# Kernel tuning notes

Measured on AMD Instinct MI355X. Metric: run time of the kernel, lower is better.

The kernel has to match this reference:

```python
import jax, jax.numpy as jnp
import numpy as np

N_NODES = 100000
N_FEATS = 2048
HIDDEN = 64
N_LABELS = 40
NNZ_FEAT = 2500000   # ~25 nonzero features per node
N_EDGES = 1600000    # avg degree 16 (directed COO entries)


def setup_inputs() -> dict:
    key = jax.random.key(0)
    ks = jax.random.split(key, 10)

    # sparse feature matrix [N_NODES, N_FEATS] in COO form
    f_rows = jax.random.randint(ks[0], (NNZ_FEAT,), 0, N_NODES)
    f_cols = jax.random.randint(ks[1], (NNZ_FEAT,), 0, N_FEATS)
    feature_indices = jnp.stack([f_rows, f_cols]).astype(jnp.int64)
    feature_values = jax.random.uniform(ks[2], (NNZ_FEAT,), dtype=jnp.float32)

    # random graph edges + self loops, then D^-1/2 (A+I) D^-1/2 normalization
    e_rows = jax.random.randint(ks[3], (N_EDGES,), 0, N_NODES)
    e_cols = jax.random.randint(ks[4], (N_EDGES,), 0, N_NODES)
    loops = jnp.arange(N_NODES)
    rows = jnp.concatenate([e_rows, loops])
    cols = jnp.concatenate([e_cols, loops])
    deg = jax.ops.segment_sum(jnp.ones_like(rows, dtype=jnp.float32), rows,
                              num_segments=N_NODES)
    deg = deg + jax.ops.segment_sum(jnp.ones_like(cols, dtype=jnp.float32), cols,
                                    num_segments=N_NODES)
    d_inv_sqrt = jax.lax.rsqrt(jnp.maximum(deg * 0.5, 1.0))
    edge_indices = jnp.stack([rows, cols]).astype(jnp.int64)
    edge_weights = d_inv_sqrt[rows] * d_inv_sqrt[cols]

    # xavier-uniform weights, uniform(-1/sqrt(out), 1/sqrt(out)) biases
    lim1 = np.sqrt(6.0 / (N_FEATS + HIDDEN))
    W1 = jax.random.uniform(ks[5], (N_FEATS, HIDDEN), jnp.float32, -lim1, lim1)
    b1 = jax.random.uniform(ks[6], (HIDDEN,), jnp.float32,
                            -1.0 / np.sqrt(HIDDEN), 1.0 / np.sqrt(HIDDEN))
    lim2 = np.sqrt(6.0 / (HIDDEN + N_LABELS))
    W2 = jax.random.uniform(ks[7], (HIDDEN, N_LABELS), jnp.float32, -lim2, lim2)
    b2 = jax.random.uniform(ks[8], (N_LABELS,), jnp.float32,
                            -1.0 / np.sqrt(N_LABELS), 1.0 / np.sqrt(N_LABELS))

    return {"feature_indices": feature_indices, "feature_values": feature_values,
            "edge_indices": edge_indices, "edge_weights": edge_weights,
            "W1": W1, "b1": b1, "W2": W2, "b2": b2}


def _spmm(rows, cols, vals, dense):
    # (sparse [N, M]) @ (dense [M, D]) -> [N, D]
    return jax.ops.segment_sum(vals[:, None] * dense[cols], rows,
                               num_segments=N_NODES)


def reference(feature_indices, feature_values, edge_indices, edge_weights,
              W1, b1, W2, b2):
    f_rows, f_cols = feature_indices
    e_rows, e_cols = edge_indices

    # layer 1: sparse feature SpMM + bias
    h = _spmm(f_rows, f_cols, feature_values, W1) + b1        # [N, HIDDEN]
    # propagate with normalized adjacency, relu (dropout is identity in eval)
    h = jax.nn.relu(_spmm(e_rows, e_cols, edge_weights, h))   # [N, HIDDEN]
    # layer 2: dense linear
    z = h @ W2 + b2                                           # [N, N_LABELS]
    # propagate again
    z = _spmm(e_rows, e_cols, edge_weights, z)                # [N, N_LABELS]
    return jax.nn.log_softmax(z, axis=1)
```

## Files before the change

kernel.cpp:

```cpp
#include <hip/hip_runtime.h>
#include <hip/hip_bf16.h>


#define HID 64
#define LAB 40
#define RSH 9
#define KMAX 512
#define TILE_A 7168
#define EPT 7

typedef __attribute__((ext_vector_type(8))) short short8;
typedef __attribute__((ext_vector_type(4))) float f32x4;

__device__ __forceinline__ float loadF(const void* p, size_t i, int bf16) {
    if (bf16) return __bfloat162float(((const __hip_bfloat16*)p)[i]);
    return ((const float*)p)[i];
}

__device__ __forceinline__ int loadI(const void* p, size_t i, int i64) {
    if (i64) return (int)(((const long long*)p)[i]);
    return ((const int*)p)[i];
}

__device__ __forceinline__ float bflo(unsigned v) { return __uint_as_float(v << 16); }
__device__ __forceinline__ float bfhi(unsigned v) { return __uint_as_float(v & 0xFFFF0000u); }
__device__ __forceinline__ unsigned bfr16(float x) {
    unsigned u = __float_as_uint(x);
    return (u + 0x7FFFu + ((u >> 16) & 1u)) >> 16;
}
__device__ __forceinline__ unsigned bfpack(float lo, float hi) {
    return bfr16(lo) | (bfr16(hi) << 16);
}

__device__ __forceinline__ unsigned fp8pack4(float a, float b, float c, float d) {
    int r = __builtin_amdgcn_cvt_pk_fp8_f32(a, b, 0, false);
    r = __builtin_amdgcn_cvt_pk_fp8_f32(c, d, r, true);
    return (unsigned)r;
}

__device__ __forceinline__ void ntload(const int2* P, int idx, int* c, float* w) {
    long long raw = __builtin_nontemporal_load((const long long*)P + idx);
    *c = (int)(unsigned)(raw & 0xFFFFFFFFll);
    *w = __int_as_float((int)(raw >> 32));
}

__device__ __forceinline__ short8 cvt8(uint2 u) {
    short8 r;
    r[0] = (short)bfr16(__builtin_amdgcn_cvt_f32_fp8((int)u.x, 0));
    r[1] = (short)bfr16(__builtin_amdgcn_cvt_f32_fp8((int)u.x, 1));
    r[2] = (short)bfr16(__builtin_amdgcn_cvt_f32_fp8((int)u.x, 2));
    r[3] = (short)bfr16(__builtin_amdgcn_cvt_f32_fp8((int)u.x, 3));
    r[4] = (short)bfr16(__builtin_amdgcn_cvt_f32_fp8((int)u.y, 0));
    r[5] = (short)bfr16(__builtin_amdgcn_cvt_f32_fp8((int)u.y, 1));
    r[6] = (short)bfr16(__builtin_amdgcn_cvt_f32_fp8((int)u.y, 2));
    r[7] = (short)bfr16(__builtin_amdgcn_cvt_f32_fp8((int)u.y, 3));
    return r;
}

__global__ void probe_kernel(const void* b1p, const void* fidxp, int* flags) {
    if (threadIdx.x == 0 && blockIdx.x == 0) {
        const unsigned short* u = (const unsigned short*)b1p;
        int bf16 = 1;
        for (int i = 0; i < 64; i += 2)
            if ((unsigned short)(u[i] & 0x7FFF) >= 0x3E80) { bf16 = 0; break; }
        const int* ip = (const int*)fidxp;
        int i64 = 1;
        for (int i = 1; i < 128; i += 2)
            if (ip[i] != 0) { i64 = 0; break; }
        flags[0] = bf16; flags[1] = i64; flags[2] = 0; flags[3] = 0;
    }
}

__global__ void zero_kernel(int4* p, int n4) {
    int i = blockIdx.x * blockDim.x + threadIdx.x;
    if (i < n4) p[i] = make_int4(0, 0, 0, 0);
}

__global__ void convw1_kernel(const void* W1, uint2* w1q, const int* flags, int ne) {
    int i = blockIdx.x * blockDim.x + threadIdx.x;
    if (i < ne) {
        float f0 = loadF(W1, (size_t)4 * i,     flags[0]);
        float f1 = loadF(W1, (size_t)4 * i + 1, flags[0]);
        float f2 = loadF(W1, (size_t)4 * i + 2, flags[0]);
        float f3 = loadF(W1, (size_t)4 * i + 3, flags[0]);
        w1q[i] = make_uint2(bfpack(f0, f1), bfpack(f2, f3));
    }
}

__global__ void convw2_kernel(const void* W2, uint4* w2f, const int* flags) {
    int tid = threadIdx.x;
    if (tid < 384) {
        int t    = tid >> 7;
        int kh   = (tid >> 6) & 1;
        int lane = tid & 63;
        int col  = t * 16 + (lane & 15);
        int kb   = kh * 32 + (lane >> 4) * 8;
        unsigned d[4];
#pragma unroll
        for (int q = 0; q < 8; q += 2) {
            float v0 = (col < LAB) ? loadF(W2, (size_t)(kb + q) * LAB + col, flags[0]) : 0.f;
            float v1 = (col < LAB) ? loadF(W2, (size_t)(kb + q + 1) * LAB + col, flags[0]) : 0.f;
            d[q >> 1] = bfpack(v0, v1);
        }
        w2f[(t * 2 + kh) * 64 + lane] = make_uint4(d[0], d[1], d[2], d[3]);
    }
}

__global__ __launch_bounds__(1024)
void histB_kernel(const void* fidx, const void* eidx, int* cntB, int* cntPB,
                  const int* flags, int nnz, int nE, int N, int nblk) {
    __shared__ int lh[KMAX];
    if (threadIdx.x < KMAX) lh[threadIdx.x] = 0;
    __syncthreads();
    const int i64 = flags[1];
    const int nT = nnz + nE;
    const int base = blockIdx.x * TILE_A;
#pragma unroll
    for (int k = 0; k < EPT; k++) {
        int i = base + k * 1024 + threadIdx.x;
        if (i < nT) {
            int grow = (i < nnz) ? loadI(fidx, (size_t)i, i64)
                                 : N + loadI(eidx, (size_t)(i - nnz), i64);
            atomicAdd(&lh[grow >> RSH], 1);
        }
    }
    __syncthreads();
    if (threadIdx.x < KMAX) {
        int c = lh[threadIdx.x];
        cntPB[(size_t)threadIdx.x * nblk + blockIdx.x] = c;
        if (c) atomicAdd(&cntB[threadIdx.x], c);
    }
}

__global__ void scanB_kernel(const int* cntB, int* bqstart, int K) {
    __shared__ int s[KMAX];
    int t = threadIdx.x;
    int x = (t < K) ? cntB[t] : 0;
    s[t] = x;
    __syncthreads();
    for (int off = 1; off < KMAX; off <<= 1) {
        int v = (t >= off) ? s[t - off] : 0;
        __syncthreads();
        s[t] += v;
        __syncthreads();
    }
    if (t < K) bqstart[t] = s[t] - x;
}

__global__ __launch_bounds__(1024)
void scanPB_kernel(int* cntPB, const int* bqstart, int nblk) {
    __shared__ int s[1024];
    const int b = blockIdx.x;
    const int t = threadIdx.x;
    int x = (t < nblk) ? cntPB[(size_t)b * nblk + t] : 0;
    s[t] = x;
    __syncthreads();
    for (int off = 1; off < 1024; off <<= 1) {
        int v = (t >= off) ? s[t - off] : 0;
        __syncthreads();
        s[t] += v;
        __syncthreads();
    }
    if (t < nblk) cntPB[(size_t)b * nblk + t] = bqstart[b] + s[t] - x;
}

__global__ __launch_bounds__(1024)
void bucketA_kernel(const void* fidx, const void* fval,
                    const void* eidx, const void* ew,
                    const int* flags, const int* cntPB, int2* Q,
                    int nnz, int nE, int N, int nblk) {
    __shared__ int2 stage[TILE_A];
    __shared__ int hist[KMAX];
    __shared__ int lofs[KMAX + 1];
    __shared__ int delta[KMAX];
    const int i64 = flags[1], bf16 = flags[0];
    const int nT = nnz + nE;
    const int base = blockIdx.x * TILE_A;
    const int t = threadIdx.x;
    if (t < KMAX) hist[t] = 0;
    __syncthreads();

    int key[EPT]; float val[EPT]; int bk[EPT]; int rk[EPT];
#pragma unroll
    for (int k = 0; k < EPT; k++) {
        int i = base + k * 1024 + t;
        bk[k] = -1; rk[k] = 0; key[k] = 0; val[k] = 0.f;
        if (i < nT) {
            int grow, c; float v;
            if (i < nnz) {
                grow = loadI(fidx, (size_t)i, i64);
                c    = loadI(fidx, (size_t)nnz + i, i64);
                v    = loadF(fval, (size_t)i, bf16);
            } else {
                int j = i - nnz;
                grow = N + loadI(eidx, (size_t)j, i64);
                c    = loadI(eidx, (size_t)nE + j, i64);
                v    = loadF(ew, (size_t)j, bf16);
            }
            int b = grow >> RSH;
            bk[k]  = b;
            key[k] = ((grow & ((1 << RSH) - 1)) << 17) | c;
            val[k] = v;
            rk[k]  = atomicAdd(&hist[b], 1);
        }
    }
    __syncthreads();

    int cnt = (t < KMAX) ? hist[t] : 0;
    if (t < KMAX) delta[t] = cnt;
    __syncthreads();
    for (int off2 = 1; off2 < KMAX; off2 <<= 1) {
        int v2 = (t >= off2 && t < KMAX) ? delta[t - off2] : 0;
        __syncthreads();
        if (t < KMAX) delta[t] += v2;
        __syncthreads();
    }
    if (t < KMAX) {
        int incl = delta[t];
        int excl = incl - cnt;
        lofs[t] = excl;
        if (t == KMAX - 1) lofs[KMAX] = incl;
        delta[t] = cntPB[(size_t)t * nblk + blockIdx.x] - excl;
    }
    __syncthreads();

#pragma unroll
    for (int k = 0; k < EPT; k++) {
        if (bk[k] >= 0)
            stage[lofs[bk[k]] + rk[k]] = make_int2(key[k], __float_as_int(val[k]));
    }
    __syncthreads();

    const int total = min(TILE_A, nT - base);
    for (int p = t; p < total; p += 1024) {
        int b = 0;
#pragma unroll
        for (int step = KMAX / 2; step; step >>= 1)
            if (lofs[b + step] <= p) b += step;
        Q[delta[b] + p] = stage[p];
    }
}

__global__ __launch_bounds__(1024)
void bucketB_kernel(const int2* Q, const int* bqstart, int* rp,
                    int2* P, int nT, int K) {
    __shared__ int lh[1 << RSH];
    __shared__ int s[1 << RSH];
    __shared__ int lstart[1 << RSH];
    const int b = blockIdx.x;
    const int t = threadIdx.x;
    const int start = bqstart[b];
    const int end = (b == K - 1) ? nT : bqstart[b + 1];
    if (t < (1 << RSH)) lh[t] = 0;
    __syncthreads();
    for (int i = start + t; i < end; i += 1024)
        atomicAdd(&lh[((unsigned)Q[i].x) >> 17], 1);
    __syncthreads();
    int x = (t < (1 << RSH)) ? lh[t] : 0;
    if (t < (1 << RSH)) s[t] = x;
    __syncthreads();
    for (int off = 1; off < (1 << RSH); off <<= 1) {
        int v = (t >= off && t < (1 << RSH)) ? s[t - off] : 0;
        __syncthreads();
        if (t < (1 << RSH)) s[t] += v;
        __syncthreads();
    }
    if (t < (1 << RSH)) {
        int rowstart = start + s[t] - x;
        rp[(b << RSH) + t] = rowstart;
        lstart[t] = rowstart;
        lh[t] = 0;
    }
    __syncthreads();
    for (int i = start + t; i < end; i += 1024) {
        int2 el = Q[i];
        int lr = ((unsigned)el.x) >> 17;
        int rank = atomicAdd(&lh[lr], 1);
        P[lstart[lr] + rank] = make_int2(el.x & 0x1FFFF, el.y);
    }
}

__global__ void gather_feat_kernel(const int* rp, const int2* P,
                                   const uint2* w1q, const void* b1,
                                   unsigned* hF8, const int* flags, int N) {
    int bf16 = flags[0];
    int wave = (blockIdx.x * blockDim.x + threadIdx.x) >> 6;
    int lane = threadIdx.x & 63;
    int g = lane >> 4, gl = lane & 15;
    int row = 4 * wave + g;
    int s = 0, e = 0;
    if (row < N) { s = rp[row]; e = rp[row + 1]; }
    float a0 = loadF(b1, (size_t)4 * gl,     bf16);
    float a1 = loadF(b1, (size_t)4 * gl + 1, bf16);
    float a2 = loadF(b1, (size_t)4 * gl + 2, bf16);
    float a3 = loadF(b1, (size_t)4 * gl + 3, bf16);
    const int sb = g << 4;
    for (int base = s; base < e; base += 16) {
        int idx = base + gl;
        int cl = 0; float vl = 0.f;
        if (idx < e) ntload(P, idx, &cl, &vl);
        int cnt = min(16, e - base);
        int j = 0;
        for (; j + 4 <= cnt; j += 4) {
            int   c0 = __shfl(cl, sb + j),     c1 = __shfl(cl, sb + j + 1);
            int   c2 = __shfl(cl, sb + j + 2), c3 = __shfl(cl, sb + j + 3);
            float v0 = __shfl(vl, sb + j),     v1 = __shfl(vl, sb + j + 1);
            float v2 = __shfl(vl, sb + j + 2), v3 = __shfl(vl, sb + j + 3);
            uint2 u0 = w1q[c0 * 16 + gl];
            uint2 u1 = w1q[c1 * 16 + gl];
            uint2 u2 = w1q[c2 * 16 + gl];
            uint2 u3 = w1q[c3 * 16 + gl];
            a0 += v0 * bflo(u0.x); a1 += v0 * bfhi(u0.x);
            a2 += v0 * bflo(u0.y); a3 += v0 * bfhi(u0.y);
            a0 += v1 * bflo(u1.x); a1 += v1 * bfhi(u1.x);
            a2 += v1 * bflo(u1.y); a3 += v1 * bfhi(u1.y);
            a0 += v2 * bflo(u2.x); a1 += v2 * bfhi(u2.x);
            a2 += v2 * bflo(u2.y); a3 += v2 * bfhi(u2.y);
            a0 += v3 * bflo(u3.x); a1 += v3 * bfhi(u3.x);
            a2 += v3 * bflo(u3.y); a3 += v3 * bfhi(u3.y);
        }
        for (; j < cnt; j++) {
            int   c = __shfl(cl, sb + j);
            float v = __shfl(vl, sb + j);
            uint2 u = w1q[c * 16 + gl];
            a0 += v * bflo(u.x); a1 += v * bfhi(u.x);
            a2 += v * bflo(u.y); a3 += v * bfhi(u.y);
        }
    }
    if (row < N) hF8[row * 16 + gl] = fp8pack4(a0, a1, a2, a3);
}

__global__ void gather_edge_h2_kernel(const int* rp, const int2* P,
                                      const unsigned* hF8, unsigned* h2F8,
                                      int N) {
    int wave = (blockIdx.x * blockDim.x + threadIdx.x) >> 6;
    int lane = threadIdx.x & 63;
    int g = lane >> 4, gl = lane & 15;
    int row = 4 * wave + g;
    int s = 0, e = 0;
    if (row < N) { s = rp[N + row]; e = rp[N + row + 1]; }
    float a0 = 0.f, a1 = 0.f, a2 = 0.f, a3 = 0.f;
    const int sb = g << 4;
    for (int base = s; base < e; base += 16) {
        int idx = base + gl;
        int cl = 0; float wl = 0.f;
        if (idx < e) ntload(P, idx, &cl, &wl);
        int cnt = min(16, e - base);
        int j = 0;
        for (; j + 8 <= cnt; j += 8) {
            int   c0 = __shfl(cl, sb + j),     c1 = __shfl(cl, sb + j + 1);
            int   c2 = __shfl(cl, sb + j + 2), c3 = __shfl(cl, sb + j + 3);
            int   c4 = __shfl(cl, sb + j + 4), c5 = __shfl(cl, sb + j + 5);
            int   c6 = __shfl(cl, sb + j + 6), c7 = __shfl(cl, sb + j + 7);
            float w0 = __shfl(wl, sb + j),     w1 = __shfl(wl, sb + j + 1);
            float w2 = __shfl(wl, sb + j + 2), w3 = __shfl(wl, sb + j + 3);
            float w4 = __shfl(wl, sb + j + 4), w5 = __shfl(wl, sb + j + 5);
            float w6 = __shfl(wl, sb + j + 6), w7 = __shfl(wl, sb + j + 7);
            int u0 = (int)hF8[c0 * 16 + gl];
            int u1 = (int)hF8[c1 * 16 + gl];
            int u2 = (int)hF8[c2 * 16 + gl];
            int u3 = (int)hF8[c3 * 16 + gl];
            int u4 = (int)hF8[c4 * 16 + gl];
            int u5 = (int)hF8[c5 * 16 + gl];
            int u6 = (int)hF8[c6 * 16 + gl];
            int u7 = (int)hF8[c7 * 16 + gl];
            a0 += w0 * __builtin_amdgcn_cvt_f32_fp8(u0, 0);
            a1 += w0 * __builtin_amdgcn_cvt_f32_fp8(u0, 1);
            a2 += w0 * __builtin_amdgcn_cvt_f32_fp8(u0, 2);
            a3 += w0 * __builtin_amdgcn_cvt_f32_fp8(u0, 3);
            a0 += w1 * __builtin_amdgcn_cvt_f32_fp8(u1, 0);
            a1 += w1 * __builtin_amdgcn_cvt_f32_fp8(u1, 1);
            a2 += w1 * __builtin_amdgcn_cvt_f32_fp8(u1, 2);
            a3 += w1 * __builtin_amdgcn_cvt_f32_fp8(u1, 3);
            a0 += w2 * __builtin_amdgcn_cvt_f32_fp8(u2, 0);
            a1 += w2 * __builtin_amdgcn_cvt_f32_fp8(u2, 1);
            a2 += w2 * __builtin_amdgcn_cvt_f32_fp8(u2, 2);
            a3 += w2 * __builtin_amdgcn_cvt_f32_fp8(u2, 3);
            a0 += w3 * __builtin_amdgcn_cvt_f32_fp8(u3, 0);
            a1 += w3 * __builtin_amdgcn_cvt_f32_fp8(u3, 1);
            a2 += w3 * __builtin_amdgcn_cvt_f32_fp8(u3, 2);
            a3 += w3 * __builtin_amdgcn_cvt_f32_fp8(u3, 3);
            a0 += w4 * __builtin_amdgcn_cvt_f32_fp8(u4, 0);
            a1 += w4 * __builtin_amdgcn_cvt_f32_fp8(u4, 1);
            a2 += w4 * __builtin_amdgcn_cvt_f32_fp8(u4, 2);
            a3 += w4 * __builtin_amdgcn_cvt_f32_fp8(u4, 3);
            a0 += w5 * __builtin_amdgcn_cvt_f32_fp8(u5, 0);
            a1 += w5 * __builtin_amdgcn_cvt_f32_fp8(u5, 1);
            a2 += w5 * __builtin_amdgcn_cvt_f32_fp8(u5, 2);
            a3 += w5 * __builtin_amdgcn_cvt_f32_fp8(u5, 3);
            a0 += w6 * __builtin_amdgcn_cvt_f32_fp8(u6, 0);
            a1 += w6 * __builtin_amdgcn_cvt_f32_fp8(u6, 1);
            a2 += w6 * __builtin_amdgcn_cvt_f32_fp8(u6, 2);
            a3 += w6 * __builtin_amdgcn_cvt_f32_fp8(u6, 3);
            a0 += w7 * __builtin_amdgcn_cvt_f32_fp8(u7, 0);
            a1 += w7 * __builtin_amdgcn_cvt_f32_fp8(u7, 1);
            a2 += w7 * __builtin_amdgcn_cvt_f32_fp8(u7, 2);
            a3 += w7 * __builtin_amdgcn_cvt_f32_fp8(u7, 3);
        }
        for (; j < cnt; j++) {
            int   c = __shfl(cl, sb + j);
            float w = __shfl(wl, sb + j);
            int u = (int)hF8[c * 16 + gl];
            a0 += w * __builtin_amdgcn_cvt_f32_fp8(u, 0);
            a1 += w * __builtin_amdgcn_cvt_f32_fp8(u, 1);
            a2 += w * __builtin_amdgcn_cvt_f32_fp8(u, 2);
            a3 += w * __builtin_amdgcn_cvt_f32_fp8(u, 3);
        }
    }
    if (row < N)
        h2F8[row * 16 + gl] = fp8pack4(fmaxf(a0, 0.f), fmaxf(a1, 0.f),
                                       fmaxf(a2, 0.f), fmaxf(a3, 0.f));
}

__global__ void dense_mfma_kernel(const unsigned* h2F8, const uint4* w2f,
                                  const void* b2, unsigned char* zb,
                                  const int* flags, int N) {
    int bf16 = flags[0];
    int wid  = (int)((blockIdx.x * blockDim.x + threadIdx.x) >> 6);
    int lane = threadIdx.x & 63;
    int ntiles = (N + 15) >> 4;
    if (wid >= ntiles) return;
    const int g = lane >> 4;
    const int fr = lane & 15;

    int arow = wid * 16 + fr;
    const uint2* hrow = (const uint2*)(h2F8 + (size_t)arow * 16);
    short8 af0 = cvt8(hrow[g]);
    short8 af1 = cvt8(hrow[4 + g]);

    f32x4 acc[3];
#pragma unroll
    for (int t = 0; t < 3; t++) {
        int col = t * 16 + fr;
        float bias = (col < LAB) ? loadF(b2, (size_t)col, bf16) : 0.f;
        acc[t][0] = bias; acc[t][1] = bias; acc[t][2] = bias; acc[t][3] = bias;
        uint4 b0 = w2f[(t * 2 + 0) * 64 + lane];
        uint4 b1 = w2f[(t * 2 + 1) * 64 + lane];
        acc[t] = __builtin_amdgcn_mfma_f32_16x16x32_bf16(
            af0, *(short8*)&b0, acc[t], 0, 0, 0);
        acc[t] = __builtin_amdgcn_mfma_f32_16x16x32_bf16(
            af1, *(short8*)&b1, acc[t], 0, 0, 0);
    }

#pragma unroll
    for (int t = 0; t < 3; t++) {
        int col = t * 16 + fr;
        if (col < LAB) {
#pragma unroll
            for (int q = 0; q < 4; q++) {
                int orow = wid * 16 + g * 4 + q;
                if (orow < N) {
                    int pk = __builtin_amdgcn_cvt_pk_fp8_f32(acc[t][q], acc[t][q], 0, false);
                    zb[(size_t)orow * LAB + col] = (unsigned char)(pk & 0xFF);
                }
            }
        }
    }
}

__global__ void gather_edge_lsm_kernel(const int* rp, const int2* P,
                                       const unsigned* zF8, void* out,
                                       const int* flags, int N) {
    int bf16 = flags[0];
    int wave = (blockIdx.x * blockDim.x + threadIdx.x) >> 6;
    int lane = threadIdx.x & 63;
    int g = lane >> 4, gl = lane & 15;
    int row = 4 * wave + g;
    int s = 0, e = 0;
    if (row < N) { s = rp[N + row]; e = rp[N + row + 1]; }
    float a0 = 0.f, a1 = 0.f, a2 = 0.f, a3 = 0.f;
    const int sb = g << 4;
    const int act = (gl < 10);
    for (int base = s; base < e; base += 16) {
        int idx = base + gl;
        int cl = 0; float wl = 0.f;
        if (idx < e) ntload(P, idx, &cl, &wl);
        int cnt = min(16, e - base);
        int j = 0;
        for (; j + 4 <= cnt; j += 4) {
            int   c0 = __shfl(cl, sb + j),     c1 = __shfl(cl, sb + j + 1);
            int   c2 = __shfl(cl, sb + j + 2), c3 = __shfl(cl, sb + j + 3);
            float w0 = __shfl(wl, sb + j),     w1 = __shfl(wl, sb + j + 1);
            float w2 = __shfl(wl, sb + j + 2), w3 = __shfl(wl, sb + j + 3);
            if (act) {
                int u0 = (int)zF8[c0 * 10 + gl];
                int u1 = (int)zF8[c1 * 10 + gl];
                int u2 = (int)zF8[c2 * 10 + gl];
                int u3 = (int)zF8[c3 * 10 + gl];
                a0 += w0 * __builtin_amdgcn_cvt_f32_fp8(u0, 0);
                a1 += w0 * __builtin_amdgcn_cvt_f32_fp8(u0, 1);
                a2 += w0 * __builtin_amdgcn_cvt_f32_fp8(u0, 2);
                a3 += w0 * __builtin_amdgcn_cvt_f32_fp8(u0, 3);
                a0 += w1 * __builtin_amdgcn_cvt_f32_fp8(u1, 0);
                a1 += w1 * __builtin_amdgcn_cvt_f32_fp8(u1, 1);
                a2 += w1 * __builtin_amdgcn_cvt_f32_fp8(u1, 2);
                a3 += w1 * __builtin_amdgcn_cvt_f32_fp8(u1, 3);
                a0 += w2 * __builtin_amdgcn_cvt_f32_fp8(u2, 0);
                a1 += w2 * __builtin_amdgcn_cvt_f32_fp8(u2, 1);
                a2 += w2 * __builtin_amdgcn_cvt_f32_fp8(u2, 2);
                a3 += w2 * __builtin_amdgcn_cvt_f32_fp8(u2, 3);
                a0 += w3 * __builtin_amdgcn_cvt_f32_fp8(u3, 0);
                a1 += w3 * __builtin_amdgcn_cvt_f32_fp8(u3, 1);
                a2 += w3 * __builtin_amdgcn_cvt_f32_fp8(u3, 2);
                a3 += w3 * __builtin_amdgcn_cvt_f32_fp8(u3, 3);
            }
        }
        for (; j < cnt; j++) {
            int   c = __shfl(cl, sb + j);
            float w = __shfl(wl, sb + j);
            if (act) {
                int u = (int)zF8[c * 10 + gl];
                a0 += w * __builtin_amdgcn_cvt_f32_fp8(u, 0);
                a1 += w * __builtin_amdgcn_cvt_f32_fp8(u, 1);
                a2 += w * __builtin_amdgcn_cvt_f32_fp8(u, 2);
                a3 += w * __builtin_amdgcn_cvt_f32_fp8(u, 3);
            }
        }
    }
    float m = act ? fmaxf(fmaxf(a0, a1), fmaxf(a2, a3)) : -INFINITY;
#pragma unroll
    for (int off = 8; off; off >>= 1) m = fmaxf(m, __shfl_xor(m, off));
    float es = act ? (__expf(a0 - m) + __expf(a1 - m) + __expf(a2 - m) + __expf(a3 - m)) : 0.f;
#pragma unroll
    for (int off = 8; off; off >>= 1) es += __shfl_xor(es, off);
    float lse = m + __logf(es);
    if (act && row < N) {
        float o0 = a0 - lse, o1 = a1 - lse, o2 = a2 - lse, o3 = a3 - lse;
        if (bf16) {
            ((uint2*)out)[(size_t)row * 10 + gl] =
                make_uint2(bfpack(o0, o1), bfpack(o2, o3));
        } else {
            float4 v = make_float4(o0, o1, o2, o3);
            ((float4*)out)[(size_t)row * 10 + gl] = v;
        }
    }
}

extern "C" void kernel_launch(void* const* d_in, const int* in_sizes, int n_in,
                              void* d_out, int out_size, void* d_ws, size_t ws_size,
                              hipStream_t stream) {
    const void* fidx = d_in[0];
    const void* fval = d_in[1];
    const void* eidx = d_in[2];
    const void* ew   = d_in[3];
    const void* W1   = d_in[4];
    const void* b1   = d_in[5];
    const void* W2   = d_in[6];
    const void* b2   = d_in[7];

    const int nnz = in_sizes[1];
    const int nW1 = in_sizes[4];
    const int nE  = in_sizes[3];
    const int N   = out_size / LAB;
    const int M   = 2 * N;
    const int nT  = nnz + nE;
    const int K   = (M + (1 << RSH) - 1) >> RSH;
    const int NBLK = (nT + TILE_A - 1) / TILE_A;

    auto align256 = [](size_t x) { return (x + 255) & ~(size_t)255; };
    char* ws = (char*)d_ws;
    size_t off = 0;
    int*   flags   = (int*)(ws + off);   off += 256;
    char*  front   = ws + off;
    unsigned* hF8  = (unsigned*)front;
    unsigned* h2F8 = hF8 + (size_t)N * 16;
    unsigned char* zb = (unsigned char*)(h2F8 + (size_t)N * 16);
    size_t frontBytes = (size_t)N * (64 + 64 + 40);
    size_t qBytes     = (size_t)nT * 8;
    off += align256(frontBytes > qBytes ? frontBytes : qBytes);
    int2*  P       = (int2*)(ws + off);  off += align256((size_t)nT * 8);
    int*   rp      = (int*)(ws + off);   off += align256(((size_t)KMAX << RSH) * 4 + 16);
    uint2* w1q     = (uint2*)(ws + off); off += align256((size_t)nW1 * 2);
    uint4* w2f     = (uint4*)(ws + off); off += align256((size_t)384 * 16);
    int*   cntB    = (int*)(ws + off);   off += KMAX * 4;
    int*   bqstart = (int*)(ws + off);   off += KMAX * 4;
    int*   cntPB   = (int*)(ws + off);   off += align256((size_t)KMAX * NBLK * 4);
    int2*  Q       = (int2*)front;

    probe_kernel<<<1, 64, 0, stream>>>(b1, fidx, flags);

    zero_kernel<<<1, 256, 0, stream>>>((int4*)cntB, KMAX / 4);
    convw1_kernel<<<(nW1 / 4 + 255) / 256, 256, 0, stream>>>(W1, w1q, flags, nW1 / 4);
    convw2_kernel<<<1, 384, 0, stream>>>(W2, w2f, flags);

    histB_kernel<<<NBLK, 1024, 0, stream>>>(fidx, eidx, cntB, cntPB,
                                            flags, nnz, nE, N, NBLK);

    scanB_kernel<<<1, KMAX, 0, stream>>>(cntB, bqstart, K);

    scanPB_kernel<<<K, 1024, 0, stream>>>(cntPB, bqstart, NBLK);

    bucketA_kernel<<<NBLK, 1024, 0, stream>>>(fidx, fval, eidx, ew, flags,
                                              cntPB, Q, nnz, nE, N, NBLK);

    bucketB_kernel<<<K, 1024, 0, stream>>>(Q, bqstart, rp, P, nT, K);

    int nwaves = (N + 3) / 4;
    int gblocks = (int)(((size_t)nwaves * 64 + 255) / 256);
    gather_feat_kernel<<<gblocks, 256, 0, stream>>>(rp, P, w1q, b1, hF8, flags, N);

    gather_edge_h2_kernel<<<gblocks, 256, 0, stream>>>(rp, P, hF8, h2F8, N);

    int ntiles = (N + 15) / 16;
    int dblocks = (int)(((size_t)ntiles * 64 + 255) / 256);
    dense_mfma_kernel<<<dblocks, 256, 0, stream>>>(h2F8, w2f, b2, zb, flags, N);

    gather_edge_lsm_kernel<<<gblocks, 256, 0, stream>>>(rp, P, (const unsigned*)zb,
                                                        d_out, flags, N);
}
```

Measured before the change: 304.1 us.

## Halve rows per bucket and stage bucketB scatter in LDS for coalesced writes

Bucket granularity drops from 512 to 256 rows, so there are 1024 buckets and each 1024-thread block handles one bucket per thread without guards. Tile size per block shrinks to 6144 elements. bucketB now scatters each bucket's elements into a shared-memory staging buffer and then writes them to P contiguously. This replaces random global scatters with coalesced stores, and buckets larger than the buffer capacity fall back to direct scatter. The trade-off is a larger prefix scan over 1024 buckets, more blocks, and a big LDS allocation that limits occupancy in bucketB.

```diff
diff --git a/kernel.cpp b/kernel.cpp
--- a/kernel.cpp
+++ b/kernel.cpp
@@ -4,10 +4,12 @@
 
 #define HID 64
 #define LAB 40
-#define RSH 9
-#define KMAX 512
-#define TILE_A 7168
-#define EPT 7
+#define RSH 8
+#define RPB (1 << RSH)
+#define KMAX 1024
+#define TILE_A 6144
+#define EPT 6
+#define CAPB 6912
 
 typedef __attribute__((ext_vector_type(8))) short short8;
 typedef __attribute__((ext_vector_type(4))) float f32x4;
@@ -110,7 +112,7 @@
 void histB_kernel(const void* fidx, const void* eidx, int* cntB, int* cntPB,
                   const int* flags, int nnz, int nE, int N, int nblk) {
     __shared__ int lh[KMAX];
-    if (threadIdx.x < KMAX) lh[threadIdx.x] = 0;
+    lh[threadIdx.x] = 0;
     __syncthreads();
     const int i64 = flags[1];
     const int nT = nnz + nE;
@@ -125,14 +127,15 @@
         }
     }
     __syncthreads();
-    if (threadIdx.x < KMAX) {
+    {
         int c = lh[threadIdx.x];
         cntPB[(size_t)threadIdx.x * nblk + blockIdx.x] = c;
         if (c) atomicAdd(&cntB[threadIdx.x], c);
     }
 }
 
-__global__ void scanB_kernel(const int* cntB, int* bqstart, int K) {
+__global__ __launch_bounds__(1024)
+void scanB_kernel(const int* cntB, int* bqstart, int K) {
     __shared__ int s[KMAX];
     int t = threadIdx.x;
     int x = (t < K) ? cntB[t] : 0;
@@ -177,7 +180,7 @@
     const int nT = nnz + nE;
     const int base = blockIdx.x * TILE_A;
     const int t = threadIdx.x;
-    if (t < KMAX) hist[t] = 0;
+    hist[t] = 0;
     __syncthreads();
 
     int key[EPT]; float val[EPT]; int bk[EPT]; int rk[EPT];
@@ -199,23 +202,23 @@
             }
             int b = grow >> RSH;
             bk[k]  = b;
-            key[k] = ((grow & ((1 << RSH) - 1)) << 17) | c;
+            key[k] = ((grow & (RPB - 1)) << 17) | c;
             val[k] = v;
             rk[k]  = atomicAdd(&hist[b], 1);
         }
     }
     __syncthreads();
 
-    int cnt = (t < KMAX) ? hist[t] : 0;
-    if (t < KMAX) delta[t] = cnt;
+    int cnt = hist[t];
+    delta[t] = cnt;
     __syncthreads();
     for (int off2 = 1; off2 < KMAX; off2 <<= 1) {
-        int v2 = (t >= off2 && t < KMAX) ? delta[t - off2] : 0;
-        __syncthreads();
-        if (t < KMAX) delta[t] += v2;
-        __syncthreads();
-    }
-    if (t < KMAX) {
+        int v2 = (t >= off2) ? delta[t - off2] : 0;
+        __syncthreads();
+        delta[t] += v2;
+        __syncthreads();
+    }
+    {
         int incl = delta[t];
         int excl = incl - cnt;
         lofs[t] = excl;
@@ -244,39 +247,53 @@
 __global__ __launch_bounds__(1024)
 void bucketB_kernel(const int2* Q, const int* bqstart, int* rp,
                     int2* P, int nT, int K) {
-    __shared__ int lh[1 << RSH];
-    __shared__ int s[1 << RSH];
-    __shared__ int lstart[1 << RSH];
+    __shared__ int2 stg[CAPB];
+    __shared__ int lh[RPB];
+    __shared__ int s[RPB];
+    __shared__ int lstart[RPB];
     const int b = blockIdx.x;
     const int t = threadIdx.x;
     const int start = bqstart[b];
     const int end = (b == K - 1) ? nT : bqstart[b + 1];
-    if (t < (1 << RSH)) lh[t] = 0;
+    const int cnt = end - start;
+    if (t < RPB) lh[t] = 0;
     __syncthreads();
     for (int i = start + t; i < end; i += 1024)
         atomicAdd(&lh[((unsigned)Q[i].x) >> 17], 1);
     __syncthreads();
-    int x = (t < (1 << RSH)) ? lh[t] : 0;
-    if (t < (1 << RSH)) s[t] = x;
-    __syncthreads();
-    for (int off = 1; off < (1 << RSH); off <<= 1) {
-        int v = (t >= off && t < (1 << RSH)) ? s[t - off] : 0;
-        __syncthreads();
-        if (t < (1 << RSH)) s[t] += v;
-        __syncthreads();
-    }
-    if (t < (1 << RSH)) {
-        int rowstart = start + s[t] - x;
-        rp[(b << RSH) + t] = rowstart;
-        lstart[t] = rowstart;
+    int x = (t < RPB) ? lh[t] : 0;
+    if (t < RPB) s[t] = x;
+    __syncthreads();
+    for (int off = 1; off < RPB; off <<= 1) {
+        int v = (t >= off && t < RPB) ? s[t - off] : 0;
+        __syncthreads();
+        if (t < RPB) s[t] += v;
+        __syncthreads();
+    }
+    if (t < RPB) {
+        int excl = s[t] - x;
+        rp[(b << RSH) + t] = start + excl;
+        lstart[t] = excl;
         lh[t] = 0;
     }
     __syncthreads();
-    for (int i = start + t; i < end; i += 1024) {
-        int2 el = Q[i];
-        int lr = ((unsigned)el.x) >> 17;
-        int rank = atomicAdd(&lh[lr], 1);
-        P[lstart[lr] + rank] = make_int2(el.x & 0x1FFFF, el.y);
+    if (cnt <= CAPB) {
+        for (int i = start + t; i < end; i += 1024) {
+            int2 el = Q[i];
+            int lr = ((unsigned)el.x) >> 17;
+            int rank = atomicAdd(&lh[lr], 1);
+            stg[lstart[lr] + rank] = make_int2(el.x & 0x1FFFF, el.y);
+        }
+        __syncthreads();
+        for (int p = t; p < cnt; p += 1024)
+            P[start + p] = stg[p];
+    } else {
+        for (int i = start + t; i < end; i += 1024) {
+            int2 el = Q[i];
+            int lr = ((unsigned)el.x) >> 17;
+            int rank = atomicAdd(&lh[lr], 1);
+            P[start + lstart[lr] + rank] = make_int2(el.x & 0x1FFFF, el.y);
+        }
     }
 }
 
@@ -554,7 +571,7 @@
     const int N   = out_size / LAB;
     const int M   = 2 * N;
     const int nT  = nnz + nE;
-    const int K   = (M + (1 << RSH) - 1) >> RSH;
+    const int K   = (M + RPB - 1) >> RSH;
     const int NBLK = (nT + TILE_A - 1) / TILE_A;
 
     auto align256 = [](size_t x) { return (x + 255) & ~(size_t)255; };
```

Measured after the change: 278.4 us. 1.09x faster.
